# Kernel optimization log

Measured on AMD Instinct MI355X. Metric: run time of the kernel, lower is better.

The kernel has to match this reference:

```python
import jax, jax.numpy as jnp
import numpy as np
import math

D_MODEL = 1024
N_HEAD = 16
FFN_HIDDEN = 4096
EPS = 1e-12


def _layernorm(x, gamma, beta):
    # faithful to repo: unbiased std (ddof=1), divide by (std + eps)
    mean = jnp.mean(x, axis=-1, keepdims=True)
    std = jnp.std(x, axis=-1, keepdims=True, ddof=1)
    return gamma * ((x - mean) / (std + EPS)) + beta


def setup_inputs() -> dict:
    key = jax.random.key(0)
    ks = jax.random.split(key, 12)
    B, L, D, H = 2, 2048, D_MODEL, FFN_HIDDEN
    s = 0.02
    inp = {
        "x": jax.random.normal(ks[0], (B, L, D), dtype=jnp.float32),
        "src_mask": jnp.ones((B, 1, 1, L), dtype=jnp.int32),
        "wq_w": jax.random.normal(ks[1], (D, D), jnp.float32) * s,
        "wq_b": jnp.zeros((D,), jnp.float32),
        "wk_w": jax.random.normal(ks[2], (D, D), jnp.float32) * s,
        "wk_b": jnp.zeros((D,), jnp.float32),
        "wv_w": jax.random.normal(ks[3], (D, D), jnp.float32) * s,
        "wv_b": jnp.zeros((D,), jnp.float32),
        "wo_w": jax.random.normal(ks[4], (D, D), jnp.float32) * s,
        "wo_b": jnp.zeros((D,), jnp.float32),
        "gamma1": jnp.ones((D,), jnp.float32),
        "beta1": jnp.zeros((D,), jnp.float32),
        "ff1_w": jax.random.normal(ks[5], (D, H), jnp.float32) * s,
        "ff1_b": jnp.zeros((H,), jnp.float32),
        "ff2_w": jax.random.normal(ks[6], (H, D), jnp.float32) * s,
        "ff2_b": jnp.zeros((D,), jnp.float32),
        "gamma2": jnp.ones((D,), jnp.float32),
        "beta2": jnp.zeros((D,), jnp.float32),
    }
    return inp


def _encoder_layer(x, src_mask, wq_w, wq_b, wk_w, wk_b, wv_w, wv_b, wo_w, wo_b,
                   gamma1, beta1, ff1_w, ff1_b, ff2_w, ff2_b, gamma2, beta2):
    B, L, D = x.shape
    H = N_HEAD
    d_t = D // H
    # projections
    q = x @ wq_w + wq_b
    k = x @ wk_w + wk_b
    v = x @ wv_w + wv_b
    # faithful .view() split: reshape [B,L,D] -> [B,H,L,d_t] (no transpose)
    q = q.reshape(B, H, L, d_t)
    k = k.reshape(B, H, L, d_t)
    v = v.reshape(B, H, L, d_t)
    score = jnp.einsum("bhqd,bhkd->bhqk", q, k) / math.sqrt(d_t)
    score = jnp.where(src_mask == 0, jnp.float32(-1e-12), score)
    score = jax.nn.softmax(score, axis=-1)
    out = jnp.einsum("bhqk,bhkd->bhqd", score, v)
    out = out.reshape(B, L, D)  # faithful .view() concat
    attn = out @ wo_w + wo_b
    # residual + LN1 (dropout p=0)
    x1 = _layernorm(attn + x, gamma1, beta1)
    # FFN
    ff = jax.nn.relu(x1 @ ff1_w + ff1_b) @ ff2_w + ff2_b
    return _layernorm(ff + x1, gamma2, beta2)


def reference(x, src_mask, wq_w, wq_b, wk_w, wk_b, wv_w, wv_b, wo_w, wo_b,
              gamma1, beta1, ff1_w, ff1_b, ff2_w, ff2_b, gamma2, beta2):
    return _encoder_layer(x, src_mask, wq_w, wq_b, wk_w, wk_b, wv_w, wv_b,
                          wo_w, wo_b, gamma1, beta1, ff1_w, ff1_b, ff2_w,
                          ff2_b, gamma2, beta2)
```

## Files before the change

kernel.cpp:

```cpp
#include <hip/hip_runtime.h>
#include <hip/hip_bf16.h>
#include <cstdint>
#include <cstddef>

using bf16 = __hip_bfloat16;
typedef __attribute__((ext_vector_type(8))) short short8v;
typedef __attribute__((ext_vector_type(4))) short short4v;
typedef __attribute__((ext_vector_type(4))) float float4v;

__device__ inline float b2f(short s) {
  union { float f; uint32_t u; } z; z.u = ((uint32_t)(uint16_t)s) << 16; return z.f;
}
__device__ inline short f2b(float f) {
  bf16 h = __float2bfloat16(f);
  return *reinterpret_cast<short*>(&h);
}

typedef const __attribute__((address_space(1))) uint32_t* gas1p;
typedef __attribute__((address_space(3))) uint32_t* las3p;
__device__ inline void gload_lds16(const void* g, void* l) {
  __builtin_amdgcn_global_load_lds((gas1p)g, (las3p)l, 16, 0, 0);
}

__global__ __launch_bounds__(256) void gemm_bt(
    const bf16* __restrict__ A, const bf16* __restrict__ Bt,
    const float* __restrict__ bias, void* __restrict__ C,
    int M, int N, int K, int ldc, int relu_mode, int out_f32) {
  __shared__ __align__(16) bf16 As[128 * 32];
  __shared__ __align__(16) bf16 Bs[128 * 32];
  const int tid = threadIdx.x;
  const int w = tid >> 6, lane = tid & 63;
  const int quad = lane >> 4, l16 = lane & 15;
  const int wrow = (w >> 1) * 64, wcol = (w & 1) * 64;
  const int mbase = blockIdx.y * 128, nbase = blockIdx.x * 128;
  const int c = w * 128 + lane;
  const int row0 = c >> 2, p0 = c & 3;
  const int row1 = (c + 64) >> 2, p1 = (c + 64) & 3;

  float4v acc[4][4];
  for (int i = 0; i < 4; i++)
    for (int j = 0; j < 4; j++) acc[i][j] = (float4v){0.f, 0.f, 0.f, 0.f};

  for (int k0 = 0; k0 < K; k0 += 32) {
    __syncthreads();
    gload_lds16(A + (size_t)(mbase + row0) * K + k0 + p0 * 8, (char*)As + w * 2048);
    gload_lds16(A + (size_t)(mbase + row1) * K + k0 + p1 * 8, (char*)As + w * 2048 + 1024);
    gload_lds16(Bt + (size_t)(nbase + row0) * K + k0 + p0 * 8, (char*)Bs + w * 2048);
    gload_lds16(Bt + (size_t)(nbase + row1) * K + k0 + p1 * 8, (char*)Bs + w * 2048 + 1024);
    __syncthreads();

    short8v a[4], b[4];
    for (int mt = 0; mt < 4; mt++)
      a[mt] = *reinterpret_cast<const short8v*>(As + (wrow + mt * 16 + l16) * 32 + quad * 8);
    for (int nt = 0; nt < 4; nt++)
      b[nt] = *reinterpret_cast<const short8v*>(Bs + (wcol + nt * 16 + l16) * 32 + quad * 8);
    for (int mt = 0; mt < 4; mt++)
      for (int nt = 0; nt < 4; nt++)
        acc[mt][nt] = __builtin_amdgcn_mfma_f32_16x16x32_bf16(a[mt], b[nt], acc[mt][nt], 0, 0, 0);
  }

  for (int nt = 0; nt < 4; nt++) {
    int col = nbase + wcol + nt * 16 + l16;
    float bv = bias[col];
    for (int mt = 0; mt < 4; mt++) {
      int row = mbase + wrow + mt * 16 + quad * 4;
      for (int r = 0; r < 4; r++) {
        float v = acc[mt][nt][r] + bv;
        if (relu_mode) v = fmaxf(v, 0.f);
        size_t idx = (size_t)(row + r) * ldc + col;
        if (out_f32) ((float*)C)[idx] = v;
        else         ((short*)C)[idx] = f2b(v);
      }
    }
  }
}

__global__ __launch_bounds__(256) void gemm_pipe(
    const bf16* __restrict__ A, const bf16* __restrict__ Bt,
    float* __restrict__ C, int K, int ldc, int k_len) {
  __shared__ __align__(16) bf16 As[2][128 * 32];
  __shared__ __align__(16) bf16 Bs[2][128 * 32];
  const int tid = threadIdx.x;
  const int w = tid >> 6, lane = tid & 63;
  const int quad = lane >> 4, l16 = lane & 15;
  const int wrow = (w >> 1) * 64, wcol = (w & 1) * 64;
  const int mbase = blockIdx.y * 128, nbase = blockIdx.x * 128;
  const int srow = tid >> 1, scol = (tid & 1) * 16;

  const bf16* ag = A + (size_t)(mbase + srow) * K + blockIdx.z * k_len + scol;
  const bf16* bg = Bt + (size_t)(nbase + srow) * K + blockIdx.z * k_len + scol;

  float4v acc[4][4];
  for (int i = 0; i < 4; i++)
    for (int j = 0; j < 4; j++) acc[i][j] = (float4v){0.f, 0.f, 0.f, 0.f};

  {
    short8v a0 = *reinterpret_cast<const short8v*>(ag);
    short8v a1 = *reinterpret_cast<const short8v*>(ag + 8);
    short8v b0 = *reinterpret_cast<const short8v*>(bg);
    short8v b1 = *reinterpret_cast<const short8v*>(bg + 8);
    *reinterpret_cast<short8v*>(&As[0][srow * 32 + scol])     = a0;
    *reinterpret_cast<short8v*>(&As[0][srow * 32 + scol + 8]) = a1;
    *reinterpret_cast<short8v*>(&Bs[0][srow * 32 + scol])     = b0;
    *reinterpret_cast<short8v*>(&Bs[0][srow * 32 + scol + 8]) = b1;
  }
  __syncthreads();

  const int KT = k_len >> 5;
  for (int kt = 0; kt < KT; kt++) {
    const int pb = kt & 1;
    short8v na0, na1, nb0, nb1;
    const bool more = (kt + 1 < KT);
    if (more) {
      const bf16* ap = ag + (kt + 1) * 32;
      const bf16* bp = bg + (kt + 1) * 32;
      na0 = *reinterpret_cast<const short8v*>(ap);
      na1 = *reinterpret_cast<const short8v*>(ap + 8);
      nb0 = *reinterpret_cast<const short8v*>(bp);
      nb1 = *reinterpret_cast<const short8v*>(bp + 8);
    }

    short8v a[4], b[4];
    for (int mt = 0; mt < 4; mt++)
      a[mt] = *reinterpret_cast<const short8v*>(&As[pb][(wrow + mt * 16 + l16) * 32 + quad * 8]);
    for (int nt = 0; nt < 4; nt++)
      b[nt] = *reinterpret_cast<const short8v*>(&Bs[pb][(wcol + nt * 16 + l16) * 32 + quad * 8]);
    for (int mt = 0; mt < 4; mt++)
      for (int nt = 0; nt < 4; nt++)
        acc[mt][nt] = __builtin_amdgcn_mfma_f32_16x16x32_bf16(a[mt], b[nt], acc[mt][nt], 0, 0, 0);

    if (more) {
      *reinterpret_cast<short8v*>(&As[1 - pb][srow * 32 + scol])     = na0;
      *reinterpret_cast<short8v*>(&As[1 - pb][srow * 32 + scol + 8]) = na1;
      *reinterpret_cast<short8v*>(&Bs[1 - pb][srow * 32 + scol])     = nb0;
      *reinterpret_cast<short8v*>(&Bs[1 - pb][srow * 32 + scol + 8]) = nb1;
    }
    __syncthreads();
  }

  for (int nt = 0; nt < 4; nt++) {
    int col = nbase + wcol + nt * 16 + l16;
    for (int mt = 0; mt < 4; mt++) {
      int row = mbase + wrow + mt * 16 + quad * 4;
      for (int r = 0; r < 4; r++)
        atomicAdd(&C[(size_t)(row + r) * ldc + col], acc[mt][nt][r]);
    }
  }
}

__global__ __launch_bounds__(256) void bias_init(
    const float* __restrict__ bias, float* __restrict__ C) {
  int c = threadIdx.x * 4;
  float4 bv = *reinterpret_cast<const float4*>(bias + c);
  *reinterpret_cast<float4*>(C + (size_t)blockIdx.x * 1024 + c) = bv;
}

__global__ __launch_bounds__(256) void attn_kernel(
    const bf16* __restrict__ qkv, const int* __restrict__ mask,
    bf16* __restrict__ ao) {
  __shared__ __align__(16) short Vt[2][64 * 40];
  __shared__ __align__(16) short Pbuf[4][32 * 40];

  const int tid = threadIdx.x;
  const int w = tid >> 6, lane = tid & 63;
  const int quad = lane >> 4, l16 = lane & 15;
  const int bh = blockIdx.y, b = bh >> 4;
  const int row0 = bh * 128;
  const int qbase = blockIdx.x * 128 + w * 32;
  const int vr = tid & 31, vdb = (tid >> 5) * 8;

  short8v aq[2][2];
  for (int h = 0; h < 2; h++)
    for (int dh = 0; dh < 2; dh++) {
      int local = (qbase + h * 16 + l16) * 64 + dh * 32 + quad * 8;
      aq[h][dh] = *reinterpret_cast<const short8v*>(
          qkv + (size_t)(row0 + (local >> 10)) * 3072 + (local & 1023));
    }

  const bf16* pk[2][2];
  for (int s = 0; s < 2; s++)
    for (int dh = 0; dh < 2; dh++) {
      int local = (s * 16 + l16) * 64 + dh * 32 + quad * 8;
      pk[s][dh] = qkv + (size_t)(row0 + (local >> 10)) * 3072 + (local & 1023) + 1024;
    }
  const bf16* pv;
  {
    int local = vr * 64 + vdb;
    pv = qkv + (size_t)(row0 + (local >> 10)) * 3072 + (local & 1023) + 2048;
  }
  const int* pm = mask + b * 2048 + quad * 4;

  float4v o[2][4];
  for (int h = 0; h < 2; h++)
    for (int nt = 0; nt < 4; nt++) o[h][nt] = (float4v){0.f, 0.f, 0.f, 0.f};
  float lsum[2] = {0.f, 0.f};

  short8v kcur[2][2], vcur;
  vcur = *reinterpret_cast<const short8v*>(pv);
  for (int s = 0; s < 2; s++)
    for (int dh = 0; dh < 2; dh++)
      kcur[s][dh] = *reinterpret_cast<const short8v*>(pk[s][dh]);
  int4 mc0 = *reinterpret_cast<const int4*>(pm);
  int4 mc1 = *reinterpret_cast<const int4*>(pm + 16);
  pv += 6144; pm += 32;
  for (int s = 0; s < 2; s++)
    for (int dh = 0; dh < 2; dh++) pk[s][dh] += 6144;
  {
    short* vt = &Vt[0][0];
    for (int j = 0; j < 8; j++) vt[(vdb + j) * 40 + vr] = vcur[j];
  }
  __syncthreads();

  for (int it = 0; it < 64; it++) {
    const int pb = it & 1;
    short8v knext[2][2], vnext;
    int4 mn0, mn1;
    if (it < 63) {
      vnext = *reinterpret_cast<const short8v*>(pv);
      for (int s = 0; s < 2; s++)
        for (int dh = 0; dh < 2; dh++)
          knext[s][dh] = *reinterpret_cast<const short8v*>(pk[s][dh]);
      mn0 = *reinterpret_cast<const int4*>(pm);
      mn1 = *reinterpret_cast<const int4*>(pm + 16);
      pv += 6144; pm += 32;
      for (int s = 0; s < 2; s++)
        for (int dh = 0; dh < 2; dh++) pk[s][dh] += 6144;
    }

    float4v st[2][2];
    for (int s = 0; s < 2; s++)
      for (int h = 0; h < 2; h++) {
        float4v t = (float4v){0.f, 0.f, 0.f, 0.f};
        t = __builtin_amdgcn_mfma_f32_16x16x32_bf16(kcur[s][0], aq[h][0], t, 0, 0, 0);
        t = __builtin_amdgcn_mfma_f32_16x16x32_bf16(kcur[s][1], aq[h][1], t, 0, 0, 0);
        st[s][h] = t;
      }

    for (int h = 0; h < 2; h++)
      for (int s = 0; s < 2; s++) {
        int4 mv = s ? mc1 : mc0;
        int mm[4] = {mv.x, mv.y, mv.z, mv.w};
        short4v pkv;
        for (int r = 0; r < 4; r++) {
          float y = st[s][h][r] * 0.180336880f;
          y = fminf(fmaxf(y, -43.3f), 43.3f);
          y = (mm[r] == 0) ? -1.4427e-12f : y;
          float e = __builtin_amdgcn_exp2f(y);
          lsum[h] += e;
          pkv[r] = f2b(e);
        }
        *reinterpret_cast<short4v*>(&Pbuf[w][(h * 16 + l16) * 40 + s * 16 + quad * 4]) = pkv;
      }
    short8v pf[2];
    for (int h = 0; h < 2; h++)
      pf[h] = *reinterpret_cast<const short8v*>(&Pbuf[w][(h * 16 + l16) * 40 + quad * 8]);
    for (int nt = 0; nt < 4; nt++) {
      short8v bv = *reinterpret_cast<const short8v*>(&Vt[pb][(nt * 16 + l16) * 40 + quad * 8]);
      for (int h = 0; h < 2; h++)
        o[h][nt] = __builtin_amdgcn_mfma_f32_16x16x32_bf16(pf[h], bv, o[h][nt], 0, 0, 0);
    }

    if (it < 63) {
      short* vt = &Vt[1 - pb][0];
      for (int j = 0; j < 8; j++) vt[(vdb + j) * 40 + vr] = vnext[j];
      for (int s = 0; s < 2; s++)
        for (int dh = 0; dh < 2; dh++) kcur[s][dh] = knext[s][dh];
      mc0 = mn0; mc1 = mn1;
    }
    __syncthreads();
  }

  for (int h = 0; h < 2; h++) {
    lsum[h] += __shfl_xor(lsum[h], 16);
    lsum[h] += __shfl_xor(lsum[h], 32);
  }
  for (int h = 0; h < 2; h++)
    for (int r = 0; r < 4; r++) {
      float linv = 1.0f / __shfl(lsum[h], quad * 4 + r);
      int qg = qbase + h * 16 + quad * 4 + r;
      for (int nt = 0; nt < 4; nt++) {
        int d = nt * 16 + l16;
        ao[(size_t)bh * 131072 + (size_t)qg * 64 + d] = __float2bfloat16(o[h][nt][r] * linv);
      }
    }
}

__global__ __launch_bounds__(256) void ln_resid(
    const void* __restrict__ a, const void* __restrict__ xres,
    const float* __restrict__ gamma, const float* __restrict__ beta,
    void* __restrict__ out, int a_f32, int x_f32, int out_f32) {
  __shared__ float red[8];
  const int row = blockIdx.x, tid = threadIdx.x;
  const int w = tid >> 6, lane = tid & 63;
  const size_t base = (size_t)row * 1024;
  float v[4]; float sum = 0.f, ss = 0.f;
  for (int i = 0; i < 4; i++) {
    int c = tid + i * 256;
    float av = a_f32 ? ((const float*)a)[base + c] : b2f(((const short*)a)[base + c]);
    float xv = x_f32 ? ((const float*)xres)[base + c] : b2f(((const short*)xres)[base + c]);
    v[i] = av + xv;
    sum += v[i]; ss += v[i] * v[i];
  }
  for (int off = 1; off < 64; off <<= 1) {
    sum += __shfl_xor(sum, off);
    ss  += __shfl_xor(ss, off);
  }
  if (lane == 0) { red[w * 2] = sum; red[w * 2 + 1] = ss; }
  __syncthreads();
  sum = red[0] + red[2] + red[4] + red[6];
  ss  = red[1] + red[3] + red[5] + red[7];
  float mean = sum * (1.0f / 1024.0f);
  float var = (ss - 1024.0f * mean * mean) * (1.0f / 1023.0f);
  var = fmaxf(var, 0.f);
  float rden = 1.0f / (sqrtf(var) + 1e-12f);
  for (int i = 0; i < 4; i++) {
    int c = tid + i * 256;
    float y = gamma[c] * ((v[i] - mean) * rden) + beta[c];
    if (out_f32) ((float*)out)[base + c] = y;
    else         ((short*)out)[base + c] = f2b(y);
  }
}

__global__ __launch_bounds__(256) void transpose_k(
    const float* __restrict__ in, bf16* __restrict__ out, int R, int C) {
  __shared__ short t[32][33];
  const int tx = threadIdx.x, ty = threadIdx.y;
  const int cb = blockIdx.x * 32, rb = blockIdx.y * 32;
  for (int j = 0; j < 4; j++)
    t[ty + j * 8][tx] = f2b(in[(size_t)(rb + ty + j * 8) * C + cb + tx]);
  __syncthreads();
  for (int j = 0; j < 4; j++)
    ((short*)out)[(size_t)(cb + ty + j * 8) * R + rb + tx] = t[tx][ty + j * 8];
}

__global__ __launch_bounds__(256) void concat3(
    const float* __restrict__ a, const float* __restrict__ b,
    const float* __restrict__ c, float* __restrict__ out) {
  int i = blockIdx.x * 256 + threadIdx.x;
  float v;
  if (i < 1024)       v = a[i];
  else if (i < 2048)  v = b[i - 1024];
  else                v = c[i - 2048];
  out[i] = v;
}

__global__ __launch_bounds__(256) void cast_f32_bf16(
    const float* __restrict__ in, bf16* __restrict__ out) {
  int i0 = (blockIdx.x * 256 + threadIdx.x) * 4;
  float4 f = *reinterpret_cast<const float4*>(in + i0);
  short* o = (short*)out + i0;
  o[0] = f2b(f.x); o[1] = f2b(f.y); o[2] = f2b(f.z); o[3] = f2b(f.w);
}

extern "C" void kernel_launch(void* const* d_in, const int* in_sizes, int n_in,
                              void* d_out, int out_size, void* d_ws, size_t ws_size,
                              hipStream_t stream) {
  (void)in_sizes; (void)n_in; (void)out_size; (void)ws_size;
  const float* x    = (const float*)d_in[0];
  const int*   mask = (const int*)d_in[1];
  const float* wq_w = (const float*)d_in[2];
  const float* wq_b = (const float*)d_in[3];
  const float* wk_w = (const float*)d_in[4];
  const float* wk_b = (const float*)d_in[5];
  const float* wv_w = (const float*)d_in[6];
  const float* wv_b = (const float*)d_in[7];
  const float* wo_w = (const float*)d_in[8];
  const float* wo_b = (const float*)d_in[9];
  const float* g1   = (const float*)d_in[10];
  const float* be1  = (const float*)d_in[11];
  const float* f1w  = (const float*)d_in[12];
  const float* f1b  = (const float*)d_in[13];
  const float* f2w  = (const float*)d_in[14];
  const float* f2b_ = (const float*)d_in[15];
  const float* g2   = (const float*)d_in[16];
  const float* be2  = (const float*)d_in[17];
  float* out = (float*)d_out;
  char* ws = (char*)d_ws;

  bf16*  QKV  = (bf16*)(ws + 0);
  bf16*  Xbf  = (bf16*)(ws + 25165824);
  bf16*  AO   = (bf16*)(ws + 25165824);
  float* PROJ = (float*)(ws + 0);
  bf16*  H    = (bf16*)(ws + 0);
  bf16*  X1   = (bf16*)(ws + 33554432);
  bf16*  WT   = (bf16*)(ws + 41943040);
  float* BQKV = (float*)(ws + 48234496);

  dim3 tb(32, 8);
  cast_f32_bf16<<<dim3(4096), dim3(256), 0, stream>>>(x, Xbf);
  transpose_k<<<dim3(32, 32), tb, 0, stream>>>(wq_w, WT, 1024, 1024);
  transpose_k<<<dim3(32, 32), tb, 0, stream>>>(wk_w, WT + 1024 * 1024, 1024, 1024);
  transpose_k<<<dim3(32, 32), tb, 0, stream>>>(wv_w, WT + 2 * 1024 * 1024, 1024, 1024);
  concat3<<<dim3(12), dim3(256), 0, stream>>>(wq_b, wk_b, wv_b, BQKV);
  gemm_bt<<<dim3(24, 32), dim3(256), 0, stream>>>(Xbf, WT, BQKV, QKV, 4096, 3072, 1024, 3072, 0, 0);
  attn_kernel<<<dim3(16, 32), dim3(256), 0, stream>>>(QKV, mask, AO);
  transpose_k<<<dim3(32, 32), tb, 0, stream>>>(wo_w, WT, 1024, 1024);
  bias_init<<<dim3(4096), dim3(256), 0, stream>>>(wo_b, PROJ);
  gemm_pipe<<<dim3(8, 32, 2), dim3(256), 0, stream>>>(AO, WT, PROJ, 1024, 1024, 512);
  ln_resid<<<dim3(4096), dim3(256), 0, stream>>>(PROJ, x, g1, be1, X1, 1, 1, 0);
  transpose_k<<<dim3(128, 32), tb, 0, stream>>>(f1w, WT, 1024, 4096);
  gemm_bt<<<dim3(32, 32), dim3(256), 0, stream>>>(X1, WT, f1b, H, 4096, 4096, 1024, 4096, 1, 0);
  transpose_k<<<dim3(32, 128), tb, 0, stream>>>(f2w, WT, 4096, 1024);
  bias_init<<<dim3(4096), dim3(256), 0, stream>>>(f2b_, out);
  gemm_pipe<<<dim3(8, 32, 2), dim3(256), 0, stream>>>(H, WT, out, 4096, 1024, 2048);
  ln_resid<<<dim3(4096), dim3(256), 0, stream>>>(out, X1, g2, be2, out, 1, 0, 1);
}
```

Measured before the change: 473.2 us.

## Halve attention query tile per wave, doubling grid, and pack V transpose stores

Each wave in the attention kernel now handles 16 query rows instead of 32, so the grid doubles to 32x32 blocks and there are more blocks to spread across the compute units. The V tile transpose into shared memory now writes packed 32-bit pairs of two key rows instead of eight scalar 16-bit stores, cutting LDS store instructions. The cost is that each K/V tile is loaded from global memory by twice as many blocks, which doubles K/V traffic per query.

```diff
diff --git a/kernel.cpp b/kernel.cpp
--- a/kernel.cpp
+++ b/kernel.cpp
@@ -159,23 +159,22 @@
     const bf16* __restrict__ qkv, const int* __restrict__ mask,
     bf16* __restrict__ ao) {
   __shared__ __align__(16) short Vt[2][64 * 40];
-  __shared__ __align__(16) short Pbuf[4][32 * 40];
+  __shared__ __align__(16) short Pbuf[4][16 * 40];
 
   const int tid = threadIdx.x;
   const int w = tid >> 6, lane = tid & 63;
   const int quad = lane >> 4, l16 = lane & 15;
   const int bh = blockIdx.y, b = bh >> 4;
   const int row0 = bh * 128;
-  const int qbase = blockIdx.x * 128 + w * 32;
-  const int vr = tid & 31, vdb = (tid >> 5) * 8;
-
-  short8v aq[2][2];
-  for (int h = 0; h < 2; h++)
-    for (int dh = 0; dh < 2; dh++) {
-      int local = (qbase + h * 16 + l16) * 64 + dh * 32 + quad * 8;
-      aq[h][dh] = *reinterpret_cast<const short8v*>(
-          qkv + (size_t)(row0 + (local >> 10)) * 3072 + (local & 1023));
-    }
+  const int qbase = blockIdx.x * 64 + w * 16;
+  const int kvp = tid & 15, dg = tid >> 4;
+
+  short8v aq[2];
+  for (int dh = 0; dh < 2; dh++) {
+    int local = (qbase + l16) * 64 + dh * 32 + quad * 8;
+    aq[dh] = *reinterpret_cast<const short8v*>(
+        qkv + (size_t)(row0 + (local >> 10)) * 3072 + (local & 1023));
+  }
 
   const bf16* pk[2][2];
   for (int s = 0; s < 2; s++)
@@ -183,86 +182,91 @@
       int local = (s * 16 + l16) * 64 + dh * 32 + quad * 8;
       pk[s][dh] = qkv + (size_t)(row0 + (local >> 10)) * 3072 + (local & 1023) + 1024;
     }
-  const bf16* pv;
+  const bf16* pva;
+  const bf16* pvb;
   {
-    int local = vr * 64 + vdb;
-    pv = qkv + (size_t)(row0 + (local >> 10)) * 3072 + (local & 1023) + 2048;
+    int la = (2 * kvp) * 64 + dg * 4;
+    pva = qkv + (size_t)(row0 + (la >> 10)) * 3072 + (la & 1023) + 2048;
+    int lb = (2 * kvp + 1) * 64 + dg * 4;
+    pvb = qkv + (size_t)(row0 + (lb >> 10)) * 3072 + (lb & 1023) + 2048;
   }
   const int* pm = mask + b * 2048 + quad * 4;
 
-  float4v o[2][4];
-  for (int h = 0; h < 2; h++)
-    for (int nt = 0; nt < 4; nt++) o[h][nt] = (float4v){0.f, 0.f, 0.f, 0.f};
-  float lsum[2] = {0.f, 0.f};
-
-  short8v kcur[2][2], vcur;
-  vcur = *reinterpret_cast<const short8v*>(pv);
+  float4v o[4];
+  for (int nt = 0; nt < 4; nt++) o[nt] = (float4v){0.f, 0.f, 0.f, 0.f};
+  float lsum = 0.f;
+
+  short8v kcur[2][2];
+  short4v va, vb;
+  va = *reinterpret_cast<const short4v*>(pva);
+  vb = *reinterpret_cast<const short4v*>(pvb);
   for (int s = 0; s < 2; s++)
     for (int dh = 0; dh < 2; dh++)
       kcur[s][dh] = *reinterpret_cast<const short8v*>(pk[s][dh]);
   int4 mc0 = *reinterpret_cast<const int4*>(pm);
   int4 mc1 = *reinterpret_cast<const int4*>(pm + 16);
-  pv += 6144; pm += 32;
+  pva += 6144; pvb += 6144; pm += 32;
   for (int s = 0; s < 2; s++)
     for (int dh = 0; dh < 2; dh++) pk[s][dh] += 6144;
   {
-    short* vt = &Vt[0][0];
-    for (int j = 0; j < 8; j++) vt[(vdb + j) * 40 + vr] = vcur[j];
+    uint32_t* vt = reinterpret_cast<uint32_t*>(&Vt[0][0]);
+    for (int i = 0; i < 4; i++)
+      vt[(dg * 4 + i) * 20 + kvp] =
+          ((uint32_t)(uint16_t)vb[i] << 16) | (uint16_t)(uint16_t)va[i];
   }
   __syncthreads();
 
   for (int it = 0; it < 64; it++) {
     const int pb = it & 1;
-    short8v knext[2][2], vnext;
+    short8v knext[2][2];
+    short4v vna, vnb;
     int4 mn0, mn1;
     if (it < 63) {
-      vnext = *reinterpret_cast<const short8v*>(pv);
+      vna = *reinterpret_cast<const short4v*>(pva);
+      vnb = *reinterpret_cast<const short4v*>(pvb);
       for (int s = 0; s < 2; s++)
         for (int dh = 0; dh < 2; dh++)
           knext[s][dh] = *reinterpret_cast<const short8v*>(pk[s][dh]);
       mn0 = *reinterpret_cast<const int4*>(pm);
       mn1 = *reinterpret_cast<const int4*>(pm + 16);
-      pv += 6144; pm += 32;
+      pva += 6144; pvb += 6144; pm += 32;
       for (int s = 0; s < 2; s++)
         for (int dh = 0; dh < 2; dh++) pk[s][dh] += 6144;
     }
 
-    float4v st[2][2];
-    for (int s = 0; s < 2; s++)
-      for (int h = 0; h < 2; h++) {
-        float4v t = (float4v){0.f, 0.f, 0.f, 0.f};
-        t = __builtin_amdgcn_mfma_f32_16x16x32_bf16(kcur[s][0], aq[h][0], t, 0, 0, 0);
-        t = __builtin_amdgcn_mfma_f32_16x16x32_bf16(kcur[s][1], aq[h][1], t, 0, 0, 0);
-        st[s][h] = t;
+    float4v st[2];
+    for (int s = 0; s < 2; s++) {
+      float4v t = (float4v){0.f, 0.f, 0.f, 0.f};
+      t = __builtin_amdgcn_mfma_f32_16x16x32_bf16(kcur[s][0], aq[0], t, 0, 0, 0);
+      t = __builtin_amdgcn_mfma_f32_16x16x32_bf16(kcur[s][1], aq[1], t, 0, 0, 0);
+      st[s] = t;
+    }
+
+    for (int s = 0; s < 2; s++) {
+      int4 mv = s ? mc1 : mc0;
+      int mm[4] = {mv.x, mv.y, mv.z, mv.w};
+      short4v pkv;
+      for (int r = 0; r < 4; r++) {
+        float y = st[s][r] * 0.180336880f;
+        y = fminf(fmaxf(y, -43.3f), 43.3f);
+        y = (mm[r] == 0) ? -1.4427e-12f : y;
+        float e = __builtin_amdgcn_exp2f(y);
+        lsum += e;
+        pkv[r] = f2b(e);
       }
-
-    for (int h = 0; h < 2; h++)
-      for (int s = 0; s < 2; s++) {
-        int4 mv = s ? mc1 : mc0;
-        int mm[4] = {mv.x, mv.y, mv.z, mv.w};
-        short4v pkv;
-        for (int r = 0; r < 4; r++) {
-          float y = st[s][h][r] * 0.180336880f;
-          y = fminf(fmaxf(y, -43.3f), 43.3f);
-          y = (mm[r] == 0) ? -1.4427e-12f : y;
-          float e = __builtin_amdgcn_exp2f(y);
-          lsum[h] += e;
-          pkv[r] = f2b(e);
-        }
-        *reinterpret_cast<short4v*>(&Pbuf[w][(h * 16 + l16) * 40 + s * 16 + quad * 4]) = pkv;
-      }
-    short8v pf[2];
-    for (int h = 0; h < 2; h++)
-      pf[h] = *reinterpret_cast<const short8v*>(&Pbuf[w][(h * 16 + l16) * 40 + quad * 8]);
+      *reinterpret_cast<short4v*>(&Pbuf[w][l16 * 40 + s * 16 + quad * 4]) = pkv;
+    }
+    short8v pf = *reinterpret_cast<const short8v*>(&Pbuf[w][l16 * 40 + quad * 8]);
     for (int nt = 0; nt < 4; nt++) {
       short8v bv = *reinterpret_cast<const short8v*>(&Vt[pb][(nt * 16 + l16) * 40 + quad * 8]);
-      for (int h = 0; h < 2; h++)
-        o[h][nt] = __builtin_amdgcn_mfma_f32_16x16x32_bf16(pf[h], bv, o[h][nt], 0, 0, 0);
+      o[nt] = __builtin_amdgcn_mfma_f32_16x16x32_bf16(pf, bv, o[nt], 0, 0, 0);
     }
 
     if (it < 63) {
-      short* vt = &Vt[1 - pb][0];
-      for (int j = 0; j < 8; j++) vt[(vdb + j) * 40 + vr] = vnext[j];
+      uint32_t* vt = reinterpret_cast<uint32_t*>(&Vt[1 - pb][0]);
+      for (int i = 0; i < 4; i++)
+        vt[(dg * 4 + i) * 20 + kvp] =
+            ((uint32_t)(uint16_t)vnb[i] << 16) | (uint16_t)(uint16_t)vna[i];
       for (int s = 0; s < 2; s++)
         for (int dh = 0; dh < 2; dh++) kcur[s][dh] = knext[s][dh];
       mc0 = mn0; mc1 = mn1;
@@ -270,19 +274,16 @@
     __syncthreads();
   }
 
-  for (int h = 0; h < 2; h++) {
-    lsum[h] += __shfl_xor(lsum[h], 16);
-    lsum[h] += __shfl_xor(lsum[h], 32);
-  }
-  for (int h = 0; h < 2; h++)
-    for (int r = 0; r < 4; r++) {
-      float linv = 1.0f / __shfl(lsum[h], quad * 4 + r);
-      int qg = qbase + h * 16 + quad * 4 + r;
-      for (int nt = 0; nt < 4; nt++) {
-        int d = nt * 16 + l16;
-        ao[(size_t)bh * 131072 + (size_t)qg * 64 + d] = __float2bfloat16(o[h][nt][r] * linv);
-      }
-    }
+  lsum += __shfl_xor(lsum, 16);
+  lsum += __shfl_xor(lsum, 32);
+  for (int r = 0; r < 4; r++) {
+    float linv = 1.0f / __shfl(lsum, quad * 4 + r);
+    int qg = qbase + quad * 4 + r;
+    for (int nt = 0; nt < 4; nt++) {
+      int d = nt * 16 + l16;
+      ao[(size_t)bh * 131072 + (size_t)qg * 64 + d] = __float2bfloat16(o[nt][r] * linv);
+    }
+  }
 }
 
 __global__ __launch_bounds__(256) void ln_resid(
@@ -393,7 +394,7 @@
   transpose_k<<<dim3(32, 32), tb, 0, stream>>>(wv_w, WT + 2 * 1024 * 1024, 1024, 1024);
   concat3<<<dim3(12), dim3(256), 0, stream>>>(wq_b, wk_b, wv_b, BQKV);
   gemm_bt<<<dim3(24, 32), dim3(256), 0, stream>>>(Xbf, WT, BQKV, QKV, 4096, 3072, 1024, 3072, 0, 0);
-  attn_kernel<<<dim3(16, 32), dim3(256), 0, stream>>>(QKV, mask, AO);
+  attn_kernel<<<dim3(32, 32), dim3(256), 0, stream>>>(QKV, mask, AO);
   transpose_k<<<dim3(32, 32), tb, 0, stream>>>(wo_w, WT, 1024, 1024);
   bias_init<<<dim3(4096), dim3(256), 0, stream>>>(wo_b, PROJ);
   gemm_pipe<<<dim3(8, 32, 2), dim3(256), 0, stream>>>(AO, WT, PROJ, 1024, 1024, 512);
```

After: 579.4 us. 22.4% more time.

## Stage K tiles through swizzled LDS and pack V transpose stores as 32-bit

Applied to the files above, without the earlier changes.

In the attention kernel, each wave previously loaded the full 32x64 K tile from global memory into registers on its own. Now the block loads each K tile once into a double-buffered, XOR-swizzled LDS buffer and every wave reads its fragments from there, cutting redundant global loads by four. The V transpose into LDS now has each thread load two rows of four elements and write packed 32-bit pairs, replacing 16-bit scattered stores. In exchange it adds 8 KB of LDS per block and extra LDS reads per iteration.

```diff
diff --git a/kernel.cpp b/kernel.cpp
--- a/kernel.cpp
+++ b/kernel.cpp
@@ -159,6 +159,7 @@
     const bf16* __restrict__ qkv, const int* __restrict__ mask,
     bf16* __restrict__ ao) {
   __shared__ __align__(16) short Vt[2][64 * 40];
+  __shared__ __align__(16) short Ks[2][32 * 64];
   __shared__ __align__(16) short Pbuf[4][32 * 40];
 
   const int tid = threadIdx.x;
@@ -167,7 +168,8 @@
   const int bh = blockIdx.y, b = bh >> 4;
   const int row0 = bh * 128;
   const int qbase = blockIdx.x * 128 + w * 32;
-  const int vr = tid & 31, vdb = (tid >> 5) * 8;
+  const int kvp = tid & 15, dg = tid >> 4;
+  const int krow = tid >> 3, kc = tid & 7;
 
   short8v aq[2][2];
   for (int h = 0; h < 2; h++)
@@ -177,16 +179,18 @@
           qkv + (size_t)(row0 + (local >> 10)) * 3072 + (local & 1023));
     }
 
-  const bf16* pk[2][2];
-  for (int s = 0; s < 2; s++)
-    for (int dh = 0; dh < 2; dh++) {
-      int local = (s * 16 + l16) * 64 + dh * 32 + quad * 8;
-      pk[s][dh] = qkv + (size_t)(row0 + (local >> 10)) * 3072 + (local & 1023) + 1024;
-    }
-  const bf16* pv;
+  const bf16* pks;
   {
-    int local = vr * 64 + vdb;
-    pv = qkv + (size_t)(row0 + (local >> 10)) * 3072 + (local & 1023) + 2048;
+    int local = krow * 64 + kc * 8;
+    pks = qkv + (size_t)(row0 + (local >> 10)) * 3072 + (local & 1023) + 1024;
+  }
+  const bf16* pva;
+  const bf16* pvb;
+  {
+    int la = (2 * kvp) * 64 + dg * 4;
+    pva = qkv + (size_t)(row0 + (la >> 10)) * 3072 + (la & 1023) + 2048;
+    int lb = (2 * kvp + 1) * 64 + dg * 4;
+    pvb = qkv + (size_t)(row0 + (lb >> 10)) * 3072 + (lb & 1023) + 2048;
   }
   const int* pm = mask + b * 2048 + quad * 4;
 
@@ -195,44 +199,51 @@
     for (int nt = 0; nt < 4; nt++) o[h][nt] = (float4v){0.f, 0.f, 0.f, 0.f};
   float lsum[2] = {0.f, 0.f};
 
-  short8v kcur[2][2], vcur;
-  vcur = *reinterpret_cast<const short8v*>(pv);
-  for (int s = 0; s < 2; s++)
-    for (int dh = 0; dh < 2; dh++)
-      kcur[s][dh] = *reinterpret_cast<const short8v*>(pk[s][dh]);
+  short8v kreg;
+  short4v va, vb;
+  kreg = *reinterpret_cast<const short8v*>(pks);
+  va = *reinterpret_cast<const short4v*>(pva);
+  vb = *reinterpret_cast<const short4v*>(pvb);
   int4 mc0 = *reinterpret_cast<const int4*>(pm);
   int4 mc1 = *reinterpret_cast<const int4*>(pm + 16);
-  pv += 6144; pm += 32;
-  for (int s = 0; s < 2; s++)
-    for (int dh = 0; dh < 2; dh++) pk[s][dh] += 6144;
+  pks += 6144; pva += 6144; pvb += 6144; pm += 32;
+  *reinterpret_cast<short8v*>(&Ks[0][krow * 64 + ((kc ^ (krow & 7)) << 3)]) = kreg;
   {
-    short* vt = &Vt[0][0];
-    for (int j = 0; j < 8; j++) vt[(vdb + j) * 40 + vr] = vcur[j];
+    uint32_t* vt = reinterpret_cast<uint32_t*>(&Vt[0][0]);
+    for (int i = 0; i < 4; i++)
+      vt[(dg * 4 + i) * 20 + kvp] =
+          ((uint32_t)(uint16_t)vb[i] << 16) | (uint16_t)(uint16_t)va[i];
   }
   __syncthreads();
 
   for (int it = 0; it < 64; it++) {
     const int pb = it & 1;
-    short8v knext[2][2], vnext;
+    short8v knreg;
+    short4v vna, vnb;
     int4 mn0, mn1;
     if (it < 63) {
-      vnext = *reinterpret_cast<const short8v*>(pv);
-      for (int s = 0; s < 2; s++)
-        for (int dh = 0; dh < 2; dh++)
-          knext[s][dh] = *reinterpret_cast<const short8v*>(pk[s][dh]);
+      knreg = *reinterpret_cast<const short8v*>(pks);
+      vna = *reinterpret_cast<const short4v*>(pva);
+      vnb = *reinterpret_cast<const short4v*>(pvb);
       mn0 = *reinterpret_cast<const int4*>(pm);
       mn1 = *reinterpret_cast<const int4*>(pm + 16);
-      pv += 6144; pm += 32;
-      for (int s = 0; s < 2; s++)
-        for (int dh = 0; dh < 2; dh++) pk[s][dh] += 6144;
-    }
+      pks += 6144; pva += 6144; pvb += 6144; pm += 32;
+    }
+
+    short8v kc_[2][2];
+    for (int s = 0; s < 2; s++)
+      for (int dh = 0; dh < 2; dh++) {
+        int row = s * 16 + l16;
+        kc_[s][dh] = *reinterpret_cast<const short8v*>(
+            &Ks[pb][row * 64 + (((dh * 4 + quad) ^ (row & 7)) << 3)]);
+      }
 
     float4v st[2][2];
     for (int s = 0; s < 2; s++)
       for (int h = 0; h < 2; h++) {
         float4v t = (float4v){0.f, 0.f, 0.f, 0.f};
-        t = __builtin_amdgcn_mfma_f32_16x16x32_bf16(kcur[s][0], aq[h][0], t, 0, 0, 0);
-        t = __builtin_amdgcn_mfma_f32_16x16x32_bf16(kcur[s][1], aq[h][1], t, 0, 0, 0);
+        t = __builtin_amdgcn_mfma_f32_16x16x32_bf16(kc_[s][0], aq[h][0], t, 0, 0, 0);
+        t = __builtin_amdgcn_mfma_f32_16x16x32_bf16(kc_[s][1], aq[h][1], t, 0, 0, 0);
         st[s][h] = t;
       }
 
@@ -261,10 +272,11 @@
     }
 
     if (it < 63) {
-      short* vt = &Vt[1 - pb][0];
-      for (int j = 0; j < 8; j++) vt[(vdb + j) * 40 + vr] = vnext[j];
-      for (int s = 0; s < 2; s++)
-        for (int dh = 0; dh < 2; dh++) kcur[s][dh] = knext[s][dh];
+      *reinterpret_cast<short8v*>(&Ks[1 - pb][krow * 64 + ((kc ^ (krow & 7)) << 3)]) = knreg;
+      uint32_t* vt = reinterpret_cast<uint32_t*>(&Vt[1 - pb][0]);
+      for (int i = 0; i < 4; i++)
+        vt[(dg * 4 + i) * 20 + kvp] =
+            ((uint32_t)(uint16_t)vnb[i] << 16) | (uint16_t)(uint16_t)vna[i];
       mc0 = mn0; mc1 = mn1;
     }
     __syncthreads();
```

Result: faster. 460.7 us (-2.6%).
